# Performance work log

Hardware: AMD Instinct MI355X
Metric: run time of the kernel (lower is better)

## Reference

```python
import jax, jax.numpy as jnp
import numpy as np

B, N, D = 1, 4096, 3072
H, DH = 16, 64
INNER = H * DH  # 1024
SCALE = DH ** -0.5
EPS = 1e-5


def setup_inputs() -> dict:
    key = jax.random.key(0)
    ks = jax.random.split(key, 4)
    x = jax.random.normal(ks[0], (B, N, D), jnp.float32)
    pe = jax.random.normal(ks[1], (1, 1, N, DH // 2, 2, 2), jnp.float32)
    w_qkv = jax.random.normal(ks[2], (3 * INNER, D), jnp.float32) * 0.02
    w_out = jax.random.normal(ks[3], (D, INNER), jnp.float32) * 0.02
    ln_g = jnp.ones((D,), jnp.float32)
    ln_b = jnp.zeros((D,), jnp.float32)
    return {"x": x, "pe": pe, "w_qkv": w_qkv, "w_out": w_out, "ln_g": ln_g, "ln_b": ln_b}


def _apply_rope(t, pe):
    # t: [b,h,n,d], pe: [1,1,n,d/2,2,2] (Flux rope layout)
    b, h, n, d = t.shape
    t_ = t.reshape(b, h, n, d // 2, 1, 2)
    out = pe[..., 0] * t_[..., 0] + pe[..., 1] * t_[..., 1]  # [b,h,n,d/2,2]
    return out.reshape(b, h, n, d)


def reference(x, pe, w_qkv, w_out, ln_g, ln_b):
    # LayerNorm (norm2)
    mu = jnp.mean(x, axis=-1, keepdims=True)
    var = jnp.mean((x - mu) ** 2, axis=-1, keepdims=True)
    xn = (x - mu) / jnp.sqrt(var + EPS) * ln_g + ln_b
    # QKV projection (no bias)
    qkv = xn @ w_qkv.T  # [b,n,3*inner]
    q, k, v = jnp.split(qkv, 3, axis=-1)
    def split_heads(t):
        return t.reshape(B, N, H, DH).transpose(0, 2, 1, 3)  # b h n d
    q, k, v = split_heads(q), split_heads(k), split_heads(v)
    # RoPE on q and k (attention_aug_bbox with mask=None, aug idx = -1 -> plain rope attn)
    q = _apply_rope(q, pe)
    k = _apply_rope(k, pe)
    scores = jnp.einsum('bhqd,bhkd->bhqk', q, k) * SCALE
    attn = jax.nn.softmax(scores, axis=-1)
    o = jnp.einsum('bhqk,bhkd->bhqd', attn, v)
    o = o.transpose(0, 2, 1, 3).reshape(B, N, INNER)  # b n (h d)
    return o @ w_out.T  # [b,n,dim]
```

## Files before the change

kernel.cpp:

```cpp
#include <hip/hip_runtime.h>
#include <hip/hip_bf16.h>

typedef unsigned short u16;
typedef __attribute__((ext_vector_type(8))) short bf16x8;
typedef __attribute__((ext_vector_type(4))) float f32x4;

#define N_TOK 4096
#define DMODEL 3072
#define NH 16
#define DHEAD 64
#define INNER 1024
#define SCALE_LOG2E 0.18033688011112042f

__device__ __forceinline__ u16 f2bf(float f) {
    union { float f; unsigned u; } un; un.f = f;
    unsigned r = un.u + 0x7fffu + ((un.u >> 16) & 1u);
    return (u16)(r >> 16);
}
__device__ __forceinline__ float bf2f(u16 u) {
    union { unsigned u; float f; } x; x.u = ((unsigned)u) << 16; return x.f;
}
__device__ __forceinline__ unsigned pk2bf(float a, float b) {
    union { float f; unsigned u; } ua, ub; ua.f = a; ub.f = b;
    return __builtin_amdgcn_perm(ub.u + 0x8000u, ua.u + 0x8000u, 0x07060302u);
}
__device__ __forceinline__ void load_lds16(const u16* g, u16* l) {
    __builtin_amdgcn_global_load_lds(
        (const __attribute__((address_space(1))) unsigned int*)g,
        (__attribute__((address_space(3))) unsigned int*)l, 16, 0, 0);
}

__device__ __forceinline__ bf16x8 build_bp(unsigned u0, unsigned u1,
                                           unsigned w0, unsigned w1) {
    auto a = __builtin_amdgcn_permlane32_swap(u0, w0, false, false);
    auto b = __builtin_amdgcn_permlane16_swap(a[0], a[1], false, false);
    auto c = __builtin_amdgcn_permlane32_swap(u1, w1, false, false);
    auto d = __builtin_amdgcn_permlane16_swap(c[0], c[1], false, false);
    union { unsigned w[4]; bf16x8 v; } r;
    r.w[0] = b[0]; r.w[1] = d[0]; r.w[2] = b[1]; r.w[3] = d[1];
    return r.v;
}

__global__ __launch_bounds__(256) void ln_kernel(const float* __restrict__ x,
                                                 const float* __restrict__ g,
                                                 const float* __restrict__ b,
                                                 u16* __restrict__ xn) {
    int row = blockIdx.x;
    int tid = threadIdx.x;
    const float4* xr = (const float4*)(x + (size_t)row * DMODEL);
    float4 v[3];
    float s = 0.f, ss = 0.f;
#pragma unroll
    for (int i = 0; i < 3; ++i) {
        v[i] = xr[i * 256 + tid];
        s  += v[i].x + v[i].y + v[i].z + v[i].w;
        ss += v[i].x * v[i].x + v[i].y * v[i].y + v[i].z * v[i].z + v[i].w * v[i].w;
    }
#pragma unroll
    for (int off = 32; off; off >>= 1) {
        s  += __shfl_xor(s, off);
        ss += __shfl_xor(ss, off);
    }
    __shared__ float red[8];
    int wid = tid >> 6, lane = tid & 63;
    if (lane == 0) { red[wid] = s; red[wid + 4] = ss; }
    __syncthreads();
    s  = red[0] + red[1] + red[2] + red[3];
    ss = red[4] + red[5] + red[6] + red[7];
    float mean = s * (1.f / DMODEL);
    float var  = ss * (1.f / DMODEL) - mean * mean;
    float rstd = rsqrtf(var + 1e-5f);
    ushort4* orow = (ushort4*)(xn + (size_t)row * DMODEL);
#pragma unroll
    for (int i = 0; i < 3; ++i) {
        float4 gg = ((const float4*)g)[i * 256 + tid];
        float4 bb = ((const float4*)b)[i * 256 + tid];
        ushort4 o;
        o.x = f2bf((v[i].x - mean) * rstd * gg.x + bb.x);
        o.y = f2bf((v[i].y - mean) * rstd * gg.y + bb.y);
        o.z = f2bf((v[i].z - mean) * rstd * gg.z + bb.z);
        o.w = f2bf((v[i].w - mean) * rstd * gg.w + bb.w);
        orow[i * 256 + tid] = o;
    }
}

__global__ __launch_bounds__(256) void cvt_bf16(const float* __restrict__ in,
                                                u16* __restrict__ out, int n4) {
    int i = blockIdx.x * 256 + threadIdx.x;
    if (i < n4) {
        float4 v = ((const float4*)in)[i];
        ushort4 o;
        o.x = f2bf(v.x); o.y = f2bf(v.y); o.z = f2bf(v.z); o.w = f2bf(v.w);
        ((ushort4*)out)[i] = o;
    }
}


#define VM6 asm volatile("s_waitcnt vmcnt(6)" ::: "memory")
#define VM4 asm volatile("s_waitcnt vmcnt(4)" ::: "memory")
#define VM0 asm volatile("s_waitcnt vmcnt(0)" ::: "memory")
#define LGK8 asm volatile("s_waitcnt lgkmcnt(8)" ::: "memory")
#define NOPS ((void)0)

#define ST_A(d, h, t) do { \
    load_lds16(pA##h##0 + (size_t)(t) * 64, &lds[(d) * 16384 + (h) * 8192 + dq]); \
    load_lds16(pA##h##1 + (size_t)(t) * 64, &lds[(d) * 16384 + (h) * 8192 + dq + 512]); \
  } while (0)
#define ST_B(d, h, t) do { \
    load_lds16(pB##h##0 + (size_t)(t) * 64, &lds[32768 + (d) * 16384 + (h) * 8192 + dq]); \
    load_lds16(pB##h##1 + (size_t)(t) * 64, &lds[32768 + (d) * 16384 + (h) * 8192 + dq + 512]); \
  } while (0)

#define PHASE(d, p, STAGE, PRE, POST) do { \
    bf16x8 afr[2][2]; \
    if ((p) == 0) { \
      _Pragma("unroll") for (int nf = 0; nf < 4; ++nf) { \
        bfr[nf][0] = *(const bf16x8*)&lds[(d) * 16384 + baseB + nf * 1024 + c0]; \
        bfr[nf][1] = *(const bf16x8*)&lds[(d) * 16384 + baseB + nf * 1024 + c1]; \
      } \
    } \
    _Pragma("unroll") for (int mfl = 0; mfl < 2; ++mfl) { \
      afr[mfl][0] = *(const bf16x8*)&lds[(d) * 16384 + (p) * 4096 + mfl * 1024 + baseA + c0]; \
      afr[mfl][1] = *(const bf16x8*)&lds[(d) * 16384 + (p) * 4096 + mfl * 1024 + baseA + c1]; \
    } \
    STAGE; \
    PRE; \
    __builtin_amdgcn_s_barrier(); \
    asm volatile("s_waitcnt lgkmcnt(0)" ::: "memory"); \
    __builtin_amdgcn_sched_barrier(0); \
    __builtin_amdgcn_s_setprio(1); \
    _Pragma("unroll") for (int mfl = 0; mfl < 2; ++mfl) \
      _Pragma("unroll") for (int nf = 0; nf < 4; ++nf) { \
        acc[(p) * 2 + mfl][nf] = __builtin_amdgcn_mfma_f32_16x16x32_bf16(afr[mfl][0], bfr[nf][0], acc[(p) * 2 + mfl][nf], 0, 0, 0); \
        acc[(p) * 2 + mfl][nf] = __builtin_amdgcn_mfma_f32_16x16x32_bf16(afr[mfl][1], bfr[nf][1], acc[(p) * 2 + mfl][nf], 0, 0, 0); \
      } \
    __builtin_amdgcn_s_setprio(0); \
    POST; \
    __builtin_amdgcn_s_barrier(); \
  } while (0)

template <int CBF16>
__global__ __launch_bounds__(512, 2) void gemm256(const u16* __restrict__ A,
                                                  const u16* __restrict__ B,
                                                  void* __restrict__ C,
                                                  int M, int Nn, int K) {
    __shared__ u16 lds[65536];
    const int tid = threadIdx.x;
    const int lane = tid & 63, wid = tid >> 6;
    const int wm = wid >> 2, wn = wid & 3;
    const int l15 = lane & 15, quad = lane >> 4;
    const int sw = l15 & 7;

    int nbx = Nn >> 8;
    int cpx = gridDim.x >> 3;
    int wg = (blockIdx.x & 7) * cpx + (blockIdx.x >> 3);
    int m0 = (wg / nbx) << 8, n0 = (wg % nbx) << 8;

    const int baseA = wm * 2048 + l15 * 64;
    const int baseB = 32768 + wn * 4096 + l15 * 64;
    const int c0 = (quad ^ sw) * 8;
    const int c1 = ((4 + quad) ^ sw) * 8;
    const int dq = wid * 1024;

    const u16 *pA00, *pA01, *pA10, *pA11, *pB00, *pB01, *pB10, *pB11;
    {
        int scol = ((lane & 7) ^ (lane >> 3)) * 8;
#define MKSRC(h, j, PA, PB) { \
        int ell = (h) * 128 + (wid * 2 + (j)) * 8 + (lane >> 3); \
        int g = ell >> 6, wmh = (ell >> 5) & 1, r = ell & 31; \
        PA = A + (size_t)(m0 + wmh * 128 + g * 32 + r) * K + scol; \
        PB = B + (size_t)(n0 + ell) * K + scol; }
        MKSRC(0, 0, pA00, pB00) MKSRC(0, 1, pA01, pB01)
        MKSRC(1, 0, pA10, pB10) MKSRC(1, 1, pA11, pB11)
#undef MKSRC
    }

    f32x4 acc[8][4];
    f32x4 zero4 = {0.f, 0.f, 0.f, 0.f};
#pragma unroll
    for (int i = 0; i < 8; ++i)
#pragma unroll
        for (int j = 0; j < 4; ++j) acc[i][j] = zero4;
    bf16x8 bfr[4][2];

    ST_B(0, 0, 0); ST_B(0, 1, 0); ST_A(0, 0, 0); ST_A(0, 1, 0);
    ST_B(1, 0, 1); ST_B(1, 1, 1); ST_A(1, 0, 1);
    VM6;
    __builtin_amdgcn_s_barrier();

    const int NIT = (K >> 7) - 1;
    for (int i = 0; i < NIT; ++i) {
        int t = 2 * i;
        PHASE(0, 0, ST_A(1, 1, t + 1), LGK8, NOPS);
        PHASE(0, 1, ST_B(0, 0, t + 2), NOPS, NOPS);
        PHASE(0, 2, ST_B(0, 1, t + 2), NOPS, NOPS);
        PHASE(0, 3, ST_A(0, 0, t + 2), NOPS, VM6);
        PHASE(1, 0, ST_A(0, 1, t + 2), LGK8, NOPS);
        PHASE(1, 1, ST_B(1, 0, t + 3), NOPS, NOPS);
        PHASE(1, 2, ST_B(1, 1, t + 3), NOPS, NOPS);
        PHASE(1, 3, ST_A(1, 0, t + 3), NOPS, VM6);
    }
    {
        int T = K >> 6;
        PHASE(0, 0, ST_A(1, 1, T - 1), LGK8, NOPS);
        PHASE(0, 1, NOPS, NOPS, NOPS);
        PHASE(0, 2, NOPS, NOPS, NOPS);
        PHASE(0, 3, NOPS, NOPS, VM0);
        PHASE(1, 0, NOPS, LGK8, NOPS);
        PHASE(1, 1, NOPS, NOPS, NOPS);
        PHASE(1, 2, NOPS, NOPS, NOPS);
        PHASE(1, 3, NOPS, NOPS, NOPS);
    }

#pragma unroll
    for (int mf = 0; mf < 8; ++mf)
#pragma unroll
        for (int nf = 0; nf < 4; ++nf)
#pragma unroll
            for (int r = 0; r < 4; ++r) {
                int rr = m0 + wm * 128 + mf * 16 + quad * 4 + r;
                int cc = n0 + wn * 64 + nf * 16 + l15;
                if (CBF16)
                    ((u16*)C)[(size_t)rr * Nn + cc] = f2bf(acc[mf][nf][r]);
                else
                    ((float*)C)[(size_t)rr * Nn + cc] = acc[mf][nf][r];
            }
}

__global__ __launch_bounds__(256) void rope_qk(const u16* __restrict__ qkv,
                                               const float* __restrict__ pe,
                                               u16* __restrict__ Qr,
                                               u16* __restrict__ Kr) {
    int n = blockIdx.x;
    int tid = threadIdx.x;
    const u16* qrow = qkv + (size_t)n * DMODEL;
    const float4* pen = (const float4*)(pe + (size_t)n * 128);
#pragma unroll
    for (int it = 0; it < 2; ++it) {
        int p = it * 256 + tid;
        int h = p >> 5, i = p & 31;
        float4 w = pen[i];
        size_t obase = ((size_t)h * N_TOK + n) * DHEAD + 2 * i;
        unsigned qq = *(const unsigned*)&qrow[h * 64 + 2 * i];
        float q0 = bf2f((u16)qq), q1 = bf2f((u16)(qq >> 16));
        *(unsigned*)&Qr[obase] = pk2bf((w.x * q0 + w.y * q1) * SCALE_LOG2E,
                                       (w.z * q0 + w.w * q1) * SCALE_LOG2E);
        unsigned kk = *(const unsigned*)&qrow[INNER + h * 64 + 2 * i];
        float k0 = bf2f((u16)kk), k1 = bf2f((u16)(kk >> 16));
        *(unsigned*)&Kr[obase] = pk2bf(w.x * k0 + w.y * k1, w.z * k0 + w.w * k1);
    }
}

__global__ __launch_bounds__(256) void v_transpose(const u16* __restrict__ qkv,
                                                   u16* __restrict__ Vt) {
    __shared__ u16 t[64][65];
    int n0 = blockIdx.x * 64;
    int h = blockIdx.y;
    int tid = threadIdx.x;
#pragma unroll
    for (int it = 0; it < 4; ++it) {
        int nr = it * 16 + (tid >> 4);
        int dc = (tid & 15) * 4;
        ushort4 v = *(const ushort4*)&qkv[(size_t)(n0 + nr) * DMODEL + 2 * INNER + h * 64 + dc];
        t[dc + 0][nr] = v.x; t[dc + 1][nr] = v.y; t[dc + 2][nr] = v.z; t[dc + 3][nr] = v.w;
    }
    __syncthreads();
#pragma unroll
    for (int it = 0; it < 4; ++it) {
        int dr = it * 16 + (tid >> 4);
        int nc = (tid & 15) * 4;
        ushort4 v;
        v.x = t[dr][nc]; v.y = t[dr][nc + 1]; v.z = t[dr][nc + 2]; v.w = t[dr][nc + 3];
        *(ushort4*)&Vt[((size_t)h * 64 + dr) * N_TOK + n0 + nc] = v;
    }
}


#define FA_STAGE(d, kt) do { \
    load_lds16(&Kh[(size_t)((kt) + rbase + rowoff) * DHEAD + csw], &lds_all[(d) * 8192 + rbase * 64]); \
    load_lds16(&Kh[(size_t)((kt) + rbase + 8 + rowoff) * DHEAD + csw], &lds_all[(d) * 8192 + (rbase + 8) * 64]); \
    load_lds16(&Vh[(size_t)(rbase + rowoff) * N_TOK + (kt) + csw], &lds_all[(d) * 8192 + 4096 + rbase * 64]); \
    load_lds16(&Vh[(size_t)(rbase + 8 + rowoff) * N_TOK + (kt) + csw], &lds_all[(d) * 8192 + 4096 + (rbase + 8) * 64]); \
  } while (0)

#define FA_TILE(d, STAGE_STMT, WAIT_STMT) do { \
    bf16x8 bk[4][2], av[4][2]; \
    _Pragma("unroll") for (int tt = 0; tt < 4; ++tt) \
      _Pragma("unroll") for (int kc = 0; kc < 2; ++kc) { \
        int off = (d) * 8192 + (tt * 16 + l15) * 64 + (((kc * 4 + quad) ^ sw) * 8); \
        bk[tt][kc] = *(const bf16x8*)&lds_all[off]; \
        av[tt][kc] = *(const bf16x8*)&lds_all[off + 4096]; \
      } \
    asm volatile("s_waitcnt lgkmcnt(0)" ::: "memory"); \
    __builtin_amdgcn_sched_barrier(0); \
    __builtin_amdgcn_s_barrier(); \
    __builtin_amdgcn_sched_barrier(0); \
    STAGE_STMT; \
    _Pragma("unroll") for (int mtQ = 0; mtQ < 2; ++mtQ) { \
      f32x4 s[4]; \
      _Pragma("unroll") for (int ntK = 0; ntK < 4; ++ntK) { \
        f32x4 t0 = __builtin_amdgcn_mfma_f32_16x16x32_bf16(bk[ntK][0], aq[mtQ][0], zero4, 0, 0, 0); \
        s[ntK] = __builtin_amdgcn_mfma_f32_16x16x32_bf16(bk[ntK][1], aq[mtQ][1], t0, 0, 0, 0); \
      } \
      unsigned pw[4][2]; \
      _Pragma("unroll") for (int ntK = 0; ntK < 4; ++ntK) { \
        pw[ntK][0] = pk2bf(__builtin_amdgcn_exp2f(s[ntK][0]), __builtin_amdgcn_exp2f(s[ntK][1])); \
        pw[ntK][1] = pk2bf(__builtin_amdgcn_exp2f(s[ntK][2]), __builtin_amdgcn_exp2f(s[ntK][3])); \
      } \
      bf16x8 bp0 = build_bp(pw[0][0], pw[0][1], pw[1][0], pw[1][1]); \
      bf16x8 bp1 = build_bp(pw[2][0], pw[2][1], pw[3][0], pw[3][1]); \
      lacc[mtQ] = __builtin_amdgcn_mfma_f32_16x16x32_bf16(ones, bp0, lacc[mtQ], 0, 0, 0); \
      lacc[mtQ] = __builtin_amdgcn_mfma_f32_16x16x32_bf16(ones, bp1, lacc[mtQ], 0, 0, 0); \
      _Pragma("unroll") for (int dt = 0; dt < 4; ++dt) { \
        o[mtQ][dt] = __builtin_amdgcn_mfma_f32_16x16x32_bf16(av[dt][0], bp0, o[mtQ][dt], 0, 0, 0); \
        o[mtQ][dt] = __builtin_amdgcn_mfma_f32_16x16x32_bf16(av[dt][1], bp1, o[mtQ][dt], 0, 0, 0); \
      } \
    } \
    WAIT_STMT; \
    __builtin_amdgcn_s_barrier(); \
    __builtin_amdgcn_sched_barrier(0); \
  } while (0)

__global__ __launch_bounds__(256, 2) void flash_attn(const u16* __restrict__ Q,
                                                     const u16* __restrict__ K,
                                                     const u16* __restrict__ Vt,
                                                     u16* __restrict__ O) {
    __shared__ u16 lds_all[16384];
    int tid = threadIdx.x, lane = tid & 63, wid = tid >> 6;
    int l15 = lane & 15, quad = lane >> 4;
    int sw = l15 & 7;
    int h = blockIdx.y;
    int q0 = blockIdx.x * 128 + wid * 32;
    const u16* Qh = Q + (size_t)h * N_TOK * DHEAD;
    const u16* Kh = K + (size_t)h * N_TOK * DHEAD;
    const u16* Vh = Vt + (size_t)h * DHEAD * N_TOK;

    f32x4 zero4 = {0.f, 0.f, 0.f, 0.f};
    bf16x8 ones;
#pragma unroll
    for (int i = 0; i < 8; ++i) ones[i] = (short)0x3F80;

    bf16x8 aq[2][2];
#pragma unroll
    for (int mtQ = 0; mtQ < 2; ++mtQ)
#pragma unroll
        for (int kc = 0; kc < 2; ++kc)
            aq[mtQ][kc] = *(const bf16x8*)&Qh[(size_t)(q0 + mtQ * 16 + l15) * DHEAD + kc * 32 + quad * 8];

    f32x4 o[2][4], lacc[2];
#pragma unroll
    for (int mtQ = 0; mtQ < 2; ++mtQ) {
#pragma unroll
        for (int dt = 0; dt < 4; ++dt) o[mtQ][dt] = zero4;
        lacc[mtQ] = zero4;
    }

    int rbase = wid * 16;
    int rowoff = lane >> 3;
    int csw = ((lane & 7) ^ rowoff) * 8;

    FA_STAGE(0, 0);
    FA_STAGE(1, 64);
    VM4;
    __builtin_amdgcn_s_barrier();
    __builtin_amdgcn_sched_barrier(0);

    for (int t = 0; t < 62; t += 2) {
        FA_TILE(0, FA_STAGE(0, (t + 2) * 64), VM4);
        FA_TILE(1, FA_STAGE(1, (t + 3) * 64), VM4);
    }
    FA_TILE(0, NOPS, VM0);
    FA_TILE(1, NOPS, NOPS);

    __syncthreads();
    u16* scratch = lds_all + wid * 2048;
#pragma unroll
    for (int mtQ = 0; mtQ < 2; ++mtQ) {
        float rl = 1.f / lacc[mtQ][0];
#pragma unroll
        for (int dt = 0; dt < 4; ++dt) {
            uint2 ov;
            ov.x = pk2bf(o[mtQ][dt][0] * rl, o[mtQ][dt][1] * rl);
            ov.y = pk2bf(o[mtQ][dt][2] * rl, o[mtQ][dt][3] * rl);
            *(uint2*)&scratch[(mtQ * 16 + l15) * 64 + dt * 16 + quad * 4] = ov;
        }
    }
#pragma unroll
    for (int p = 0; p < 4; ++p) {
        int q_local = p * 8 + (lane >> 3);
        int dcol = (lane & 7) * 8;
        bf16x8 v = *(const bf16x8*)&scratch[q_local * 64 + dcol];
        *(bf16x8*)&O[(size_t)(q0 + q_local) * INNER + h * 64 + dcol] = v;
    }
}

extern "C" void kernel_launch(void* const* d_in, const int* in_sizes, int n_in,
                              void* d_out, int out_size, void* d_ws, size_t ws_size,
                              hipStream_t stream) {
    const float* x     = (const float*)d_in[0];
    const float* pe    = (const float*)d_in[1];
    const float* w_qkv = (const float*)d_in[2];
    const float* w_out = (const float*)d_in[3];
    const float* ln_g  = (const float*)d_in[4];
    const float* ln_b  = (const float*)d_in[5];
    float* out = (float*)d_out;

    char* ws = (char*)d_ws;
    u16* xn  = (u16*)ws;  ws += (size_t)N_TOK * DMODEL * 2;
    u16* wq  = (u16*)ws;  ws += (size_t)3 * INNER * DMODEL * 2;
    u16* wo  = (u16*)ws;  ws += (size_t)DMODEL * INNER * 2;
    u16* qkv = (u16*)ws;  ws += (size_t)N_TOK * DMODEL * 2;
    u16* Qr  = (u16*)ws;  ws += (size_t)NH * N_TOK * DHEAD * 2;
    u16* Kr  = (u16*)ws;  ws += (size_t)NH * N_TOK * DHEAD * 2;
    u16* Vt  = (u16*)ws;  ws += (size_t)NH * DHEAD * N_TOK * 2;
    u16* Ob  = (u16*)ws;  ws += (size_t)N_TOK * INNER * 2;

    ln_kernel<<<N_TOK, 256, 0, stream>>>(x, ln_g, ln_b, xn);
    {
        int n4 = 3 * INNER * DMODEL / 4;
        cvt_bf16<<<(n4 + 255) / 256, 256, 0, stream>>>(w_qkv, wq, n4);
    }
    {
        int n4 = DMODEL * INNER / 4;
        cvt_bf16<<<(n4 + 255) / 256, 256, 0, stream>>>(w_out, wo, n4);
    }
    gemm256<1><<<dim3((N_TOK / 256) * (DMODEL / 256)), 512, 0, stream>>>(xn, wq, qkv, N_TOK, DMODEL, DMODEL);
    rope_qk<<<N_TOK, 256, 0, stream>>>(qkv, pe, Qr, Kr);
    v_transpose<<<dim3(N_TOK / 64, NH), 256, 0, stream>>>(qkv, Vt);
    flash_attn<<<dim3(N_TOK / 128, NH), 256, 0, stream>>>(Qr, Kr, Vt, Ob);
    gemm256<0><<<dim3((N_TOK / 256) * (DMODEL / 256)), 512, 0, stream>>>(Ob, wo, out, N_TOK, DMODEL, INNER);
}
```

Measured before the change: 349.2 us.

## Merge prep and rope/transpose kernels; halve flash-attn query tile for occupancy

Merges LayerNorm and both weight conversions into one launch, and RoPE plus the V transpose into another, cutting kernel launches from eight to five. The flash attention kernel now processes 16 query rows per wave instead of 32, doubling the grid and raising the launch-bounds occupancy target from 2 to 4 blocks. Fewer rows per wave lowers register pressure and adds parallelism, but each block now reuses every K/V tile loaded into LDS across half as many queries, so K/V traffic doubles.

```diff
diff --git a/kernel.cpp b/kernel.cpp
--- a/kernel.cpp
+++ b/kernel.cpp
@@ -41,57 +41,69 @@
     return r.v;
 }
 
-__global__ __launch_bounds__(256) void ln_kernel(const float* __restrict__ x,
-                                                 const float* __restrict__ g,
-                                                 const float* __restrict__ b,
-                                                 u16* __restrict__ xn) {
-    int row = blockIdx.x;
+__global__ __launch_bounds__(256) void prep(const float* __restrict__ x,
+                                            const float* __restrict__ g,
+                                            const float* __restrict__ b,
+                                            u16* __restrict__ xn,
+                                            const float* __restrict__ w_qkv,
+                                            u16* __restrict__ wq,
+                                            const float* __restrict__ w_out,
+                                            u16* __restrict__ wo) {
+    int bid = blockIdx.x;
     int tid = threadIdx.x;
-    const float4* xr = (const float4*)(x + (size_t)row * DMODEL);
-    float4 v[3];
-    float s = 0.f, ss = 0.f;
-#pragma unroll
-    for (int i = 0; i < 3; ++i) {
-        v[i] = xr[i * 256 + tid];
-        s  += v[i].x + v[i].y + v[i].z + v[i].w;
-        ss += v[i].x * v[i].x + v[i].y * v[i].y + v[i].z * v[i].z + v[i].w * v[i].w;
-    }
-#pragma unroll
-    for (int off = 32; off; off >>= 1) {
-        s  += __shfl_xor(s, off);
-        ss += __shfl_xor(ss, off);
-    }
-    __shared__ float red[8];
-    int wid = tid >> 6, lane = tid & 63;
-    if (lane == 0) { red[wid] = s; red[wid + 4] = ss; }
-    __syncthreads();
-    s  = red[0] + red[1] + red[2] + red[3];
-    ss = red[4] + red[5] + red[6] + red[7];
-    float mean = s * (1.f / DMODEL);
-    float var  = ss * (1.f / DMODEL) - mean * mean;
-    float rstd = rsqrtf(var + 1e-5f);
-    ushort4* orow = (ushort4*)(xn + (size_t)row * DMODEL);
-#pragma unroll
-    for (int i = 0; i < 3; ++i) {
-        float4 gg = ((const float4*)g)[i * 256 + tid];
-        float4 bb = ((const float4*)b)[i * 256 + tid];
-        ushort4 o;
-        o.x = f2bf((v[i].x - mean) * rstd * gg.x + bb.x);
-        o.y = f2bf((v[i].y - mean) * rstd * gg.y + bb.y);
-        o.z = f2bf((v[i].z - mean) * rstd * gg.z + bb.z);
-        o.w = f2bf((v[i].w - mean) * rstd * gg.w + bb.w);
-        orow[i * 256 + tid] = o;
-    }
-}
-
-__global__ __launch_bounds__(256) void cvt_bf16(const float* __restrict__ in,
-                                                u16* __restrict__ out, int n4) {
-    int i = blockIdx.x * 256 + threadIdx.x;
-    if (i < n4) {
-        float4 v = ((const float4*)in)[i];
-        ushort4 o;
-        o.x = f2bf(v.x); o.y = f2bf(v.y); o.z = f2bf(v.z); o.w = f2bf(v.w);
-        ((ushort4*)out)[i] = o;
+    if (bid < 4096) {
+        int row = bid;
+        const float4* xr = (const float4*)(x + (size_t)row * DMODEL);
+        float4 v[3];
+        float s = 0.f, ss = 0.f;
+#pragma unroll
+        for (int i = 0; i < 3; ++i) {
+            v[i] = xr[i * 256 + tid];
+            s  += v[i].x + v[i].y + v[i].z + v[i].w;
+            ss += v[i].x * v[i].x + v[i].y * v[i].y + v[i].z * v[i].z + v[i].w * v[i].w;
+        }
+#pragma unroll
+        for (int off = 32; off; off >>= 1) {
+            s  += __shfl_xor(s, off);
+            ss += __shfl_xor(ss, off);
+        }
+        __shared__ float red[8];
+        int wid = tid >> 6, lane = tid & 63;
+        if (lane == 0) { red[wid] = s; red[wid + 4] = ss; }
+        __syncthreads();
+        s  = red[0] + red[1] + red[2] + red[3];
+        ss = red[4] + red[5] + red[6] + red[7];
+        float mean = s * (1.f / DMODEL);
+        float var  = ss * (1.f / DMODEL) - mean * mean;
+        float rstd = rsqrtf(var + 1e-5f);
+        ushort4* orow = (ushort4*)(xn + (size_t)row * DMODEL);
+#pragma unroll
+        for (int i = 0; i < 3; ++i) {
+            float4 gg = ((const float4*)g)[i * 256 + tid];
+            float4 bb = ((const float4*)b)[i * 256 + tid];
+            ushort4 o;
+            o.x = f2bf((v[i].x - mean) * rstd * gg.x + bb.x);
+            o.y = f2bf((v[i].y - mean) * rstd * gg.y + bb.y);
+            o.z = f2bf((v[i].z - mean) * rstd * gg.z + bb.z);
+            o.w = f2bf((v[i].w - mean) * rstd * gg.w + bb.w);
+            orow[i * 256 + tid] = o;
+        }
+    } else if (bid < 4096 + 2048) {
+        const int n4 = 3 * INNER * DMODEL / 4;
+        for (int i = (bid - 4096) * 256 + tid; i < n4; i += 2048 * 256) {
+            float4 v = ((const float4*)w_qkv)[i];
+            ushort4 o;
+            o.x = f2bf(v.x); o.y = f2bf(v.y); o.z = f2bf(v.z); o.w = f2bf(v.w);
+            ((ushort4*)wq)[i] = o;
+        }
+    } else {
+        const int n4 = DMODEL * INNER / 4;
+        for (int i = (bid - 6144) * 256 + tid; i < n4; i += 512 * 256) {
+            float4 v = ((const float4*)w_out)[i];
+            ushort4 o;
+            o.x = f2bf(v.x); o.y = f2bf(v.y); o.z = f2bf(v.z); o.w = f2bf(v.w);
+            ((ushort4*)wo)[i] = o;
+        }
     }
 }
 
@@ -227,51 +239,52 @@
             }
 }
 
-__global__ __launch_bounds__(256) void rope_qk(const u16* __restrict__ qkv,
+__global__ __launch_bounds__(256) void rope_vt(const u16* __restrict__ qkv,
                                                const float* __restrict__ pe,
                                                u16* __restrict__ Qr,
-                                               u16* __restrict__ Kr) {
-    int n = blockIdx.x;
+                                               u16* __restrict__ Kr,
+                                               u16* __restrict__ Vt) {
+    int bid = blockIdx.x;
     int tid = threadIdx.x;
-    const u16* qrow = qkv + (size_t)n * DMODEL;
-    const float4* pen = (const float4*)(pe + (size_t)n * 128);
-#pragma unroll
-    for (int it = 0; it < 2; ++it) {
-        int p = it * 256 + tid;
-        int h = p >> 5, i = p & 31;
-        float4 w = pen[i];
-        size_t obase = ((size_t)h * N_TOK + n) * DHEAD + 2 * i;
-        unsigned qq = *(const unsigned*)&qrow[h * 64 + 2 * i];
-        float q0 = bf2f((u16)qq), q1 = bf2f((u16)(qq >> 16));
-        *(unsigned*)&Qr[obase] = pk2bf((w.x * q0 + w.y * q1) * SCALE_LOG2E,
-                                       (w.z * q0 + w.w * q1) * SCALE_LOG2E);
-        unsigned kk = *(const unsigned*)&qrow[INNER + h * 64 + 2 * i];
-        float k0 = bf2f((u16)kk), k1 = bf2f((u16)(kk >> 16));
-        *(unsigned*)&Kr[obase] = pk2bf(w.x * k0 + w.y * k1, w.z * k0 + w.w * k1);
-    }
-}
-
-__global__ __launch_bounds__(256) void v_transpose(const u16* __restrict__ qkv,
-                                                   u16* __restrict__ Vt) {
-    __shared__ u16 t[64][65];
-    int n0 = blockIdx.x * 64;
-    int h = blockIdx.y;
-    int tid = threadIdx.x;
-#pragma unroll
-    for (int it = 0; it < 4; ++it) {
-        int nr = it * 16 + (tid >> 4);
-        int dc = (tid & 15) * 4;
-        ushort4 v = *(const ushort4*)&qkv[(size_t)(n0 + nr) * DMODEL + 2 * INNER + h * 64 + dc];
-        t[dc + 0][nr] = v.x; t[dc + 1][nr] = v.y; t[dc + 2][nr] = v.z; t[dc + 3][nr] = v.w;
-    }
-    __syncthreads();
-#pragma unroll
-    for (int it = 0; it < 4; ++it) {
-        int dr = it * 16 + (tid >> 4);
-        int nc = (tid & 15) * 4;
-        ushort4 v;
-        v.x = t[dr][nc]; v.y = t[dr][nc + 1]; v.z = t[dr][nc + 2]; v.w = t[dr][nc + 3];
-        *(ushort4*)&Vt[((size_t)h * 64 + dr) * N_TOK + n0 + nc] = v;
+    if (bid < 4096) {
+        int n = bid;
+        const u16* qrow = qkv + (size_t)n * DMODEL;
+        const float4* pen = (const float4*)(pe + (size_t)n * 128);
+#pragma unroll
+        for (int it = 0; it < 2; ++it) {
+            int p = it * 256 + tid;
+            int h = p >> 5, i = p & 31;
+            float4 w = pen[i];
+            size_t obase = ((size_t)h * N_TOK + n) * DHEAD + 2 * i;
+            unsigned qq = *(const unsigned*)&qrow[h * 64 + 2 * i];
+            float q0 = bf2f((u16)qq), q1 = bf2f((u16)(qq >> 16));
+            *(unsigned*)&Qr[obase] = pk2bf((w.x * q0 + w.y * q1) * SCALE_LOG2E,
+                                           (w.z * q0 + w.w * q1) * SCALE_LOG2E);
+            unsigned kk = *(const unsigned*)&qrow[INNER + h * 64 + 2 * i];
+            float k0 = bf2f((u16)kk), k1 = bf2f((u16)(kk >> 16));
+            *(unsigned*)&Kr[obase] = pk2bf(w.x * k0 + w.y * k1, w.z * k0 + w.w * k1);
+        }
+    } else {
+        __shared__ u16 t[64][65];
+        int tb = bid - 4096;
+        int n0 = (tb & 63) * 64;
+        int h = tb >> 6;
+#pragma unroll
+        for (int it = 0; it < 4; ++it) {
+            int nr = it * 16 + (tid >> 4);
+            int dc = (tid & 15) * 4;
+            ushort4 v = *(const ushort4*)&qkv[(size_t)(n0 + nr) * DMODEL + 2 * INNER + h * 64 + dc];
+            t[dc + 0][nr] = v.x; t[dc + 1][nr] = v.y; t[dc + 2][nr] = v.z; t[dc + 3][nr] = v.w;
+        }
+        __syncthreads();
+#pragma unroll
+        for (int it = 0; it < 4; ++it) {
+            int dr = it * 16 + (tid >> 4);
+            int nc = (tid & 15) * 4;
+            ushort4 v;
+            v.x = t[dr][nc]; v.y = t[dr][nc + 1]; v.z = t[dr][nc + 2]; v.w = t[dr][nc + 3];
+            *(ushort4*)&Vt[((size_t)h * 64 + dr) * N_TOK + n0 + nc] = v;
+        }
     }
 }
 
@@ -296,11 +309,11 @@
     __builtin_amdgcn_s_barrier(); \
     __builtin_amdgcn_sched_barrier(0); \
     STAGE_STMT; \
-    _Pragma("unroll") for (int mtQ = 0; mtQ < 2; ++mtQ) { \
+    { \
       f32x4 s[4]; \
       _Pragma("unroll") for (int ntK = 0; ntK < 4; ++ntK) { \
-        f32x4 t0 = __builtin_amdgcn_mfma_f32_16x16x32_bf16(bk[ntK][0], aq[mtQ][0], zero4, 0, 0, 0); \
-        s[ntK] = __builtin_amdgcn_mfma_f32_16x16x32_bf16(bk[ntK][1], aq[mtQ][1], t0, 0, 0, 0); \
+        f32x4 t0 = __builtin_amdgcn_mfma_f32_16x16x32_bf16(bk[ntK][0], aq[0], zero4, 0, 0, 0); \
+        s[ntK] = __builtin_amdgcn_mfma_f32_16x16x32_bf16(bk[ntK][1], aq[1], t0, 0, 0, 0); \
       } \
       unsigned pw[4][2]; \
       _Pragma("unroll") for (int ntK = 0; ntK < 4; ++ntK) { \
@@ -309,11 +322,11 @@
       } \
       bf16x8 bp0 = build_bp(pw[0][0], pw[0][1], pw[1][0], pw[1][1]); \
       bf16x8 bp1 = build_bp(pw[2][0], pw[2][1], pw[3][0], pw[3][1]); \
-      lacc[mtQ] = __builtin_amdgcn_mfma_f32_16x16x32_bf16(ones, bp0, lacc[mtQ], 0, 0, 0); \
-      lacc[mtQ] = __builtin_amdgcn_mfma_f32_16x16x32_bf16(ones, bp1, lacc[mtQ], 0, 0, 0); \
+      lacc = __builtin_amdgcn_mfma_f32_16x16x32_bf16(ones, bp0, lacc, 0, 0, 0); \
+      lacc = __builtin_amdgcn_mfma_f32_16x16x32_bf16(ones, bp1, lacc, 0, 0, 0); \
       _Pragma("unroll") for (int dt = 0; dt < 4; ++dt) { \
-        o[mtQ][dt] = __builtin_amdgcn_mfma_f32_16x16x32_bf16(av[dt][0], bp0, o[mtQ][dt], 0, 0, 0); \
-        o[mtQ][dt] = __builtin_amdgcn_mfma_f32_16x16x32_bf16(av[dt][1], bp1, o[mtQ][dt], 0, 0, 0); \
+        o[dt] = __builtin_amdgcn_mfma_f32_16x16x32_bf16(av[dt][0], bp0, o[dt], 0, 0, 0); \
+        o[dt] = __builtin_amdgcn_mfma_f32_16x16x32_bf16(av[dt][1], bp1, o[dt], 0, 0, 0); \
       } \
     } \
     WAIT_STMT; \
@@ -321,7 +334,7 @@
     __builtin_amdgcn_sched_barrier(0); \
   } while (0)
 
-__global__ __launch_bounds__(256, 2) void flash_attn(const u16* __restrict__ Q,
+__global__ __launch_bounds__(256, 4) void flash_attn(const u16* __restrict__ Q,
                                                      const u16* __restrict__ K,
                                                      const u16* __restrict__ Vt,
                                                      u16* __restrict__ O) {
@@ -330,7 +343,7 @@
     int l15 = lane & 15, quad = lane >> 4;
     int sw = l15 & 7;
     int h = blockIdx.y;
-    int q0 = blockIdx.x * 128 + wid * 32;
+    int q0 = blockIdx.x * 64 + wid * 16;
     const u16* Qh = Q + (size_t)h * N_TOK * DHEAD;
     const u16* Kh = K + (size_t)h * N_TOK * DHEAD;
     const u16* Vh = Vt + (size_t)h * DHEAD * N_TOK;
@@ -340,20 +353,15 @@
 #pragma unroll
     for (int i = 0; i < 8; ++i) ones[i] = (short)0x3F80;
 
-    bf16x8 aq[2][2];
-#pragma unroll
-    for (int mtQ = 0; mtQ < 2; ++mtQ)
-#pragma unroll
-        for (int kc = 0; kc < 2; ++kc)
-            aq[mtQ][kc] = *(const bf16x8*)&Qh[(size_t)(q0 + mtQ * 16 + l15) * DHEAD + kc * 32 + quad * 8];
-
-    f32x4 o[2][4], lacc[2];
-#pragma unroll
-    for (int mtQ = 0; mtQ < 2; ++mtQ) {
-#pragma unroll
-        for (int dt = 0; dt < 4; ++dt) o[mtQ][dt] = zero4;
-        lacc[mtQ] = zero4;
-    }
+    bf16x8 aq[2];
+#pragma unroll
+    for (int kc = 0; kc < 2; ++kc)
+        aq[kc] = *(const bf16x8*)&Qh[(size_t)(q0 + l15) * DHEAD + kc * 32 + quad * 8];
+
+    f32x4 o[4], lacc;
+#pragma unroll
+    for (int dt = 0; dt < 4; ++dt) o[dt] = zero4;
+    lacc = zero4;
 
     int rbase = wid * 16;
     int rowoff = lane >> 3;
@@ -373,20 +381,19 @@
     FA_TILE(1, NOPS, NOPS);
 
     __syncthreads();
-    u16* scratch = lds_all + wid * 2048;
-#pragma unroll
-    for (int mtQ = 0; mtQ < 2; ++mtQ) {
-        float rl = 1.f / lacc[mtQ][0];
+    u16* scratch = lds_all + wid * 1024;
+    {
+        float rl = 1.f / lacc[0];
 #pragma unroll
         for (int dt = 0; dt < 4; ++dt) {
             uint2 ov;
-            ov.x = pk2bf(o[mtQ][dt][0] * rl, o[mtQ][dt][1] * rl);
-            ov.y = pk2bf(o[mtQ][dt][2] * rl, o[mtQ][dt][3] * rl);
-            *(uint2*)&scratch[(mtQ * 16 + l15) * 64 + dt * 16 + quad * 4] = ov;
-        }
-    }
-#pragma unroll
-    for (int p = 0; p < 4; ++p) {
+            ov.x = pk2bf(o[dt][0] * rl, o[dt][1] * rl);
+            ov.y = pk2bf(o[dt][2] * rl, o[dt][3] * rl);
+            *(uint2*)&scratch[l15 * 64 + dt * 16 + quad * 4] = ov;
+        }
+    }
+#pragma unroll
+    for (int p = 0; p < 2; ++p) {
         int q_local = p * 8 + (lane >> 3);
         int dcol = (lane & 7) * 8;
         bf16x8 v = *(const bf16x8*)&scratch[q_local * 64 + dcol];
@@ -415,18 +422,9 @@
     u16* Vt  = (u16*)ws;  ws += (size_t)NH * DHEAD * N_TOK * 2;
     u16* Ob  = (u16*)ws;  ws += (size_t)N_TOK * INNER * 2;
 
-    ln_kernel<<<N_TOK, 256, 0, stream>>>(x, ln_g, ln_b, xn);
-    {
-        int n4 = 3 * INNER * DMODEL / 4;
-        cvt_bf16<<<(n4 + 255) / 256, 256, 0, stream>>>(w_qkv, wq, n4);
-    }
-    {
-        int n4 = DMODEL * INNER / 4;
-        cvt_bf16<<<(n4 + 255) / 256, 256, 0, stream>>>(w_out, wo, n4);
-    }
+    prep<<<4096 + 2048 + 512, 256, 0, stream>>>(x, ln_g, ln_b, xn, w_qkv, wq, w_out, wo);
     gemm256<1><<<dim3((N_TOK / 256) * (DMODEL / 256)), 512, 0, stream>>>(xn, wq, qkv, N_TOK, DMODEL, DMODEL);
-    rope_qk<<<N_TOK, 256, 0, stream>>>(qkv, pe, Qr, Kr);
-    v_transpose<<<dim3(N_TOK / 64, NH), 256, 0, stream>>>(qkv, Vt);
-    flash_attn<<<dim3(N_TOK / 128, NH), 256, 0, stream>>>(Qr, Kr, Vt, Ob);
+    rope_vt<<<4096 + 1024, 256, 0, stream>>>(qkv, pe, Qr, Kr, Vt);
+    flash_attn<<<dim3(N_TOK / 64, NH), 256, 0, stream>>>(Qr, Kr, Vt, Ob);
     gemm256<0><<<dim3((N_TOK / 256) * (DMODEL / 256)), 512, 0, stream>>>(Ob, wo, out, N_TOK, DMODEL, INNER);
 }
```

Result: no change. 352.9 us (+1.1%).
